# Performance work log

Measured on AMD Instinct MI355X. Metric: run time of the kernel, lower is better.

The kernel has to match this reference:

```python
import jax, jax.numpy as jnp
import numpy as np

LEAKY_SLOPE = 0.2
N, IN_DIM, OUT_DIM = 8192, 128, 64


def setup_inputs() -> dict:
    key = jax.random.key(0)
    k1, k2, k3, k4, k5 = jax.random.split(key, 5)
    X = jax.random.normal(k1, (N, IN_DIM), dtype=jnp.float32)
    A = jax.random.randint(k2, (N, N), 0, 2, dtype=jnp.int32)
    W = jax.random.normal(k3, (IN_DIM, OUT_DIM), dtype=jnp.float32) / np.sqrt(IN_DIM)
    a_l = jax.random.normal(k4, (OUT_DIM,), dtype=jnp.float32) / np.sqrt(OUT_DIM)
    a_r = jax.random.normal(k5, (OUT_DIM,), dtype=jnp.float32) / np.sqrt(OUT_DIM)
    return {"X": X, "A": A, "W": W, "a_l": a_l, "a_r": a_r}


def reference(X, A, W, a_l, a_r):
    # 1) linear transform: H = X @ W  -> [N, out_dim]
    H = X @ W
    # 2) additive attention scores: e_ij = leaky_relu(a_l.H_i + a_r.H_j)
    e_l = H @ a_l  # [N]
    e_r = H @ a_r  # [N]
    e = jax.nn.leaky_relu(e_l[:, None] + e_r[None, :], negative_slope=LEAKY_SLOPE)
    # 3) mask non-edges
    e = jnp.where(A == 0, -jnp.inf, e)
    # 4) row-wise softmax over neighbors j
    alpha = jax.nn.softmax(e, axis=1)
    # 5) weighted aggregation
    return alpha @ H
```

## Files before the change

### kernel.cpp

```cpp
#include <hip/hip_runtime.h>

typedef __attribute__((ext_vector_type(8))) short short8v;
typedef __attribute__((ext_vector_type(4))) float f32x4;
typedef __attribute__((ext_vector_type(2))) unsigned int uint2v;

#define NN 8192
#define HDIM 64
#define KDIM 128
#define LOG2E 1.44269504088896340736f

#if defined(__has_builtin)
#if __has_builtin(__builtin_amdgcn_cvt_pk_fp8_f32) && __has_builtin(__builtin_amdgcn_mfma_f32_16x16x32_fp8_fp8)
#define FP8PATH 1
#endif
#endif

#define PIN() asm volatile("" ::: "memory")
#define BAR() asm volatile("s_waitcnt lgkmcnt(0)\n\ts_barrier" ::: "memory")

__device__ __forceinline__ unsigned short f2b(float f) {
    unsigned int u = __float_as_uint(f);
    return (unsigned short)((u + 0x7fffu + ((u >> 16) & 1u)) >> 16);
}

__global__ __launch_bounds__(256) void gat_prep(
    const float* __restrict__ X, const float* __restrict__ W,
    const float* __restrict__ al, const float* __restrict__ ar,
    void* __restrict__ HbTv, float* __restrict__ el2p,
    float* __restrict__ cpv, float* __restrict__ erp)
{
    __shared__ float Wl[KDIM * HDIM];
    const int t = threadIdx.x;
    {
        const float4* Wv = (const float4*)W;
        float4* Wlv = (float4*)Wl;
#pragma unroll
        for (int s = 0; s < 8; ++s) Wlv[t + s * 256] = Wv[t + s * 256];
    }
    __syncthreads();
    const int row = blockIdx.x * 32 + (t >> 3);
    const int cg = t & 7;
    const int c0 = cg * 8;
    float al8[8], ar8[8];
#pragma unroll
    for (int j = 0; j < 8; ++j) { al8[j] = al[c0 + j]; ar8[j] = ar[c0 + j]; }
    float acc[8];
#pragma unroll
    for (int j = 0; j < 8; ++j) acc[j] = 0.f;
    const float4* Xv = (const float4*)(X + row * KDIM);
    for (int k4 = 0; k4 < 32; ++k4) {
        float4 x4 = Xv[k4];
        float xs[4] = {x4.x, x4.y, x4.z, x4.w};
#pragma unroll
        for (int kk = 0; kk < 4; ++kk) {
            const int k = k4 * 4 + kk;
            const float x = xs[kk];
            const float4 w0 = *(const float4*)&Wl[k * HDIM + c0];
            const float4 w1 = *(const float4*)&Wl[k * HDIM + c0 + 4];
            acc[0] = fmaf(x, w0.x, acc[0]); acc[1] = fmaf(x, w0.y, acc[1]);
            acc[2] = fmaf(x, w0.z, acc[2]); acc[3] = fmaf(x, w0.w, acc[3]);
            acc[4] = fmaf(x, w1.x, acc[4]); acc[5] = fmaf(x, w1.y, acc[5]);
            acc[6] = fmaf(x, w1.z, acc[6]); acc[7] = fmaf(x, w1.w, acc[7]);
        }
    }
    float pl = 0.f, pr = 0.f;
#pragma unroll
    for (int j = 0; j < 8; ++j) {
        pl = fmaf(acc[j], al8[j], pl);
        pr = fmaf(acc[j], ar8[j], pr);
    }
    pl += __shfl_xor(pl, 1, 64); pl += __shfl_xor(pl, 2, 64); pl += __shfl_xor(pl, 4, 64);
    pr += __shfl_xor(pr, 1, 64); pr += __shfl_xor(pr, 2, 64); pr += __shfl_xor(pr, 4, 64);
    if (cg == 0) {
        const float el = pl;
        const float s8 = el + 8.0f;
        const float m = fmaxf(s8, 0.2f * s8);
        el2p[row] = (el - m + 8.0f) * LOG2E;
        cpv[row] = (-0.8f * m + 6.4f) * LOG2E;
        erp[row] = pr * LOG2E;
    }
#ifdef FP8PATH
    unsigned char* HbT8 = (unsigned char*)HbTv;
#pragma unroll
    for (int j = 0; j < 8; ++j) {
        const unsigned int b8 =
            (unsigned int)__builtin_amdgcn_cvt_pk_fp8_f32(acc[j], acc[j], 0, false) & 0xffu;
        HbT8[(long)(c0 + j) * NN + row] = (unsigned char)b8;
    }
#else
    unsigned short* HbT = (unsigned short*)HbTv;
#pragma unroll
    for (int j = 0; j < 8; ++j) HbT[(long)(c0 + j) * NN + row] = f2b(acc[j]);
#endif
}

__global__ __launch_bounds__(256, 4) void gat_main(
    const int* __restrict__ A, const void* __restrict__ HbTv,
    const float* __restrict__ el2p, const float* __restrict__ cpv,
    const float* __restrict__ erp, float* __restrict__ out_part,
    float* __restrict__ dsum_part)
{
    const int t = threadIdx.x;
    const int l = t & 63;
    const int w = t >> 6;
    const int rowbase = (blockIdx.x >> 1) * 16;
    const int jsplit = blockIdx.x & 1;
    const int jq16 = jsplit * 16;
    const int l15 = l & 15, lq = l >> 4;

    float el2c[4], cpc[4];
    const int4* Ap[4];
#pragma unroll
    for (int i = 0; i < 4; ++i) {
        const int gr = rowbase + 4 * i + w;
        el2c[i] = el2p[gr];
        cpc[i] = cpv[gr];
        Ap[i] = (const int4*)(A + (long)gr * NN + 4 * l);
    }
    f32x4 acc = {0.f, 0.f, 0.f, 0.f};
    f32x4 accs = {0.f, 0.f, 0.f, 0.f};
    const bool do_sum = (w == 0);

    int4 A0[4], A1[4];
    float4 E0, E1;

    auto loadT = [&](int4* av, float4& e4, int jt) {
        const int jb4 = jt * 64;
#pragma unroll
        for (int i = 0; i < 4; ++i) av[i] = Ap[i][jb4];
        e4 = *(const float4*)(erp + jt * 256 + 4 * l);
    };

#ifdef FP8PATH
    __shared__ __align__(16) unsigned char plds[2][16 * 264];
    const unsigned char* bbase = (const unsigned char*)HbTv + (long)(w * 16 + l15) * NN + lq * 8;
    const int aoff = l15 * 264 + lq * 8;
    const long long ONES8 = 0x3838383838383838LL;
    unsigned long long Bf[8];

    auto issueB = [&](int jt) {
        const unsigned char* bp = bbase + (long)jt * 256;
#pragma unroll
        for (int kc = 0; kc < 8; ++kc)
            Bf[kc] = *(const unsigned long long*)(bp + kc * 32);
    };

    auto phase1 = [&](const int4* av, const float4 e4, unsigned char* buf) {
        const float e[4] = {e4.x, e4.y, e4.z, e4.w};
#pragma unroll
        for (int i = 0; i < 4; ++i) {
            const int am[4] = {av[i].x, av[i].y, av[i].z, av[i].w};
            float p[4];
#pragma unroll
            for (int c = 0; c < 4; ++c) {
                const float u = el2c[i] + e[c];
                const float v = fmaf(u, 0.2f, cpc[i]);
                float g = fmaxf(u, v);
                g = am[c] ? g : -1e30f;
                p[c] = __builtin_amdgcn_exp2f(g);
            }
            unsigned int pk = (unsigned int)__builtin_amdgcn_cvt_pk_fp8_f32(p[0], p[1], 0, false);
            pk = (unsigned int)__builtin_amdgcn_cvt_pk_fp8_f32(p[2], p[3], (int)pk, true);
            *(unsigned int*)(buf + (4 * i + w) * 264 + 4 * l) = pk;
        }
    };

    auto mfmaT = [&](const unsigned char* buf) {
        __builtin_amdgcn_s_setprio(1);
#pragma unroll
        for (int kc = 0; kc < 8; ++kc) {
            const long long af = *(const long long*)(buf + aoff + kc * 32);
            acc = __builtin_amdgcn_mfma_f32_16x16x32_fp8_fp8(af, (long long)Bf[kc], acc, 0, 0, 0);
            if (do_sum)
                accs = __builtin_amdgcn_mfma_f32_16x16x32_fp8_fp8(af, ONES8, accs, 0, 0, 0);
        }
        __builtin_amdgcn_s_setprio(0);
    };
#else
    __shared__ unsigned short plds[2][16 * 264];
    union { unsigned short s[8]; short8v v; } ones;
#pragma unroll
    for (int i = 0; i < 8; ++i) ones.s[i] = 0x3F80;
    const unsigned short* bbase = (const unsigned short*)HbTv + (long)(w * 16 + l15) * NN + lq * 8;
    const int aoff = l15 * 264 + lq * 8;
    short8v Bf[8];

    auto issueB = [&](int jt) {
        const unsigned short* bp = bbase + (long)jt * 256;
#pragma unroll
        for (int kc = 0; kc < 8; ++kc) Bf[kc] = *(const short8v*)(bp + kc * 32);
    };

    auto phase1 = [&](const int4* av, const float4 e4, unsigned short* buf) {
        const float e[4] = {e4.x, e4.y, e4.z, e4.w};
#pragma unroll
        for (int i = 0; i < 4; ++i) {
            const int am[4] = {av[i].x, av[i].y, av[i].z, av[i].w};
            float p[4];
#pragma unroll
            for (int c = 0; c < 4; ++c) {
                const float u = el2c[i] + e[c];
                const float v = fmaf(u, 0.2f, cpc[i]);
                float g = fmaxf(u, v);
                g = am[c] ? g : -1e30f;
                p[c] = __builtin_amdgcn_exp2f(g);
            }
            const unsigned int lo = (__float_as_uint(p[0]) >> 16) |
                                    (__float_as_uint(p[1]) & 0xffff0000u);
            const unsigned int hi = (__float_as_uint(p[2]) >> 16) |
                                    (__float_as_uint(p[3]) & 0xffff0000u);
            *(uint2v*)(buf + (4 * i + w) * 264 + 4 * l) = (uint2v){lo, hi};
        }
    };

    auto mfmaT = [&](const unsigned short* buf) {
        __builtin_amdgcn_s_setprio(1);
#pragma unroll
        for (int kc = 0; kc < 8; ++kc) {
            short8v af = *(const short8v*)(buf + aoff + kc * 32);
            acc = __builtin_amdgcn_mfma_f32_16x16x32_bf16(af, Bf[kc], acc, 0, 0, 0);
            if (do_sum)
                accs = __builtin_amdgcn_mfma_f32_16x16x32_bf16(af, ones.v, accs, 0, 0, 0);
        }
        __builtin_amdgcn_s_setprio(0);
    };
#endif

    loadT(A0, E0, jq16);
    loadT(A1, E1, jq16 + 1);
#pragma unroll
    for (int s = 0; s < 8; ++s) {
        const int jt = jq16 + 2 * s;
        issueB(jt);
        PIN();
        phase1(A0, E0, plds[0]);
        if (s < 7) loadT(A0, E0, jt + 2);
        BAR();
        mfmaT(plds[0]);
        issueB(jt + 1);
        PIN();
        phase1(A1, E1, plds[1]);
        if (s < 7) loadT(A1, E1, jt + 3);
        BAR();
        mfmaT(plds[1]);
    }

    if (do_sum && l15 == 0)
#pragma unroll
        for (int r = 0; r < 4; ++r)
            dsum_part[(long)jsplit * NN + rowbase + lq * 4 + r] = accs[r];
    float* op = out_part + (long)jsplit * NN * HDIM;
#pragma unroll
    for (int r = 0; r < 4; ++r) {
        const int row = lq * 4 + r;
        op[(long)(rowbase + row) * HDIM + w * 16 + l15] = acc[r];
    }
}

__global__ __launch_bounds__(256) void gat_norm(
    const float* __restrict__ out_part, const float* __restrict__ dsum_part,
    float* __restrict__ out)
{
    const int i4 = blockIdx.x * 256 + threadIdx.x;
    const int row = i4 >> 4;
    const float4* p0 = (const float4*)out_part;
    const float4 v0 = p0[i4];
    const float4 v1 = p0[i4 + (NN * HDIM / 4)];
    const float d = dsum_part[row] + dsum_part[NN + row];
    const float ri = 1.0f / d;
    float4 o;
    o.x = (v0.x + v1.x) * ri;
    o.y = (v0.y + v1.y) * ri;
    o.z = (v0.z + v1.z) * ri;
    o.w = (v0.w + v1.w) * ri;
    ((float4*)out)[i4] = o;
}

extern "C" void kernel_launch(void* const* d_in, const int* in_sizes, int n_in,
                              void* d_out, int out_size, void* d_ws, size_t ws_size,
                              hipStream_t stream) {
    const float *X = nullptr, *W = nullptr, *al = nullptr, *ar = nullptr;
    const int* A = nullptr;
    for (int i = 0; i < n_in; ++i) {
        const long s = in_sizes[i];
        if (s == (long)NN * NN) A = (const int*)d_in[i];
        else if (s == (long)NN * KDIM) X = (const float*)d_in[i];
        else if (s == (long)KDIM * HDIM) W = (const float*)d_in[i];
        else if (s == HDIM) { if (!al) al = (const float*)d_in[i]; else ar = (const float*)d_in[i]; }
    }
    float* out = (float*)d_out;
    void* HbTv = d_ws;
    float* el2p = (float*)((char*)d_ws + (long)NN * HDIM * 2);
    float* cpv = el2p + NN;
    float* erp = cpv + NN;
    float* out_part = erp + NN;
    float* dsum_part = out_part + 2L * NN * HDIM;
    hipLaunchKernelGGL(gat_prep, dim3(256), dim3(256), 0, stream, X, W, al, ar, HbTv, el2p, cpv, erp);
    hipLaunchKernelGGL(gat_main, dim3(1024), dim3(256), 0, stream, A, HbTv, el2p, cpv, erp, out_part, dsum_part);
    hipLaunchKernelGGL(gat_norm, dim3(512), dim3(256), 0, stream, out_part, dsum_part, out);
}
```

Before: 90.23 us.

## Merge two tile phases per barrier with quad-buffered LDS and dual B registers

Restructures the main loop so both phase1 computations for a tile pair run before one barrier, followed by both MFMA groups. To keep this race-free, the LDS P buffer becomes four-way rotating and the B fragments get two register sets. This halves the barriers per iteration and lets more global loads stay in flight, at the cost of twice the LDS use and more live registers, which may reduce occupancy.

```diff
diff --git a/kernel.cpp b/kernel.cpp
--- a/kernel.cpp
+++ b/kernel.cpp
@@ -132,17 +132,21 @@
     };
 
 #ifdef FP8PATH
-    __shared__ __align__(16) unsigned char plds[2][16 * 264];
+    __shared__ __align__(16) unsigned char plds[4][16 * 264];
     const unsigned char* bbase = (const unsigned char*)HbTv + (long)(w * 16 + l15) * NN + lq * 8;
     const int aoff = l15 * 264 + lq * 8;
     const long long ONES8 = 0x3838383838383838LL;
-    unsigned long long Bf[8];
-
-    auto issueB = [&](int jt) {
+    unsigned long long Bfa[8], Bfb[8];
+
+    auto issueBa = [&](int jt) {
         const unsigned char* bp = bbase + (long)jt * 256;
 #pragma unroll
-        for (int kc = 0; kc < 8; ++kc)
-            Bf[kc] = *(const unsigned long long*)(bp + kc * 32);
+        for (int kc = 0; kc < 8; ++kc) Bfa[kc] = *(const unsigned long long*)(bp + kc * 32);
+    };
+    auto issueBb = [&](int jt) {
+        const unsigned char* bp = bbase + (long)jt * 256;
+#pragma unroll
+        for (int kc = 0; kc < 8; ++kc) Bfb[kc] = *(const unsigned long long*)(bp + kc * 32);
     };
 
     auto phase1 = [&](const int4* av, const float4 e4, unsigned char* buf) {
@@ -165,30 +169,46 @@
         }
     };
 
-    auto mfmaT = [&](const unsigned char* buf) {
+    auto mfmaTa = [&](const unsigned char* buf) {
         __builtin_amdgcn_s_setprio(1);
 #pragma unroll
         for (int kc = 0; kc < 8; ++kc) {
             const long long af = *(const long long*)(buf + aoff + kc * 32);
-            acc = __builtin_amdgcn_mfma_f32_16x16x32_fp8_fp8(af, (long long)Bf[kc], acc, 0, 0, 0);
+            acc = __builtin_amdgcn_mfma_f32_16x16x32_fp8_fp8(af, (long long)Bfa[kc], acc, 0, 0, 0);
             if (do_sum)
                 accs = __builtin_amdgcn_mfma_f32_16x16x32_fp8_fp8(af, ONES8, accs, 0, 0, 0);
         }
         __builtin_amdgcn_s_setprio(0);
     };
+    auto mfmaTb = [&](const unsigned char* buf) {
+        __builtin_amdgcn_s_setprio(1);
+#pragma unroll
+        for (int kc = 0; kc < 8; ++kc) {
+            const long long af = *(const long long*)(buf + aoff + kc * 32);
+            acc = __builtin_amdgcn_mfma_f32_16x16x32_fp8_fp8(af, (long long)Bfb[kc], acc, 0, 0, 0);
+            if (do_sum)
+                accs = __builtin_amdgcn_mfma_f32_16x16x32_fp8_fp8(af, ONES8, accs, 0, 0, 0);
+        }
+        __builtin_amdgcn_s_setprio(0);
+    };
 #else
-    __shared__ unsigned short plds[2][16 * 264];
+    __shared__ unsigned short plds[4][16 * 264];
     union { unsigned short s[8]; short8v v; } ones;
 #pragma unroll
     for (int i = 0; i < 8; ++i) ones.s[i] = 0x3F80;
     const unsigned short* bbase = (const unsigned short*)HbTv + (long)(w * 16 + l15) * NN + lq * 8;
     const int aoff = l15 * 264 + lq * 8;
-    short8v Bf[8];
-
-    auto issueB = [&](int jt) {
+    short8v Bfa[8], Bfb[8];
+
+    auto issueBa = [&](int jt) {
         const unsigned short* bp = bbase + (long)jt * 256;
 #pragma unroll
-        for (int kc = 0; kc < 8; ++kc) Bf[kc] = *(const short8v*)(bp + kc * 32);
+        for (int kc = 0; kc < 8; ++kc) Bfa[kc] = *(const short8v*)(bp + kc * 32);
+    };
+    auto issueBb = [&](int jt) {
+        const unsigned short* bp = bbase + (long)jt * 256;
+#pragma unroll
+        for (int kc = 0; kc < 8; ++kc) Bfb[kc] = *(const short8v*)(bp + kc * 32);
     };
 
     auto phase1 = [&](const int4* av, const float4 e4, unsigned short* buf) {
@@ -213,17 +233,28 @@
         }
     };
 
-    auto mfmaT = [&](const unsigned short* buf) {
+    auto mfmaTa = [&](const unsigned short* buf) {
         __builtin_amdgcn_s_setprio(1);
 #pragma unroll
         for (int kc = 0; kc < 8; ++kc) {
             short8v af = *(const short8v*)(buf + aoff + kc * 32);
-            acc = __builtin_amdgcn_mfma_f32_16x16x32_bf16(af, Bf[kc], acc, 0, 0, 0);
+            acc = __builtin_amdgcn_mfma_f32_16x16x32_bf16(af, Bfa[kc], acc, 0, 0, 0);
             if (do_sum)
                 accs = __builtin_amdgcn_mfma_f32_16x16x32_bf16(af, ones.v, accs, 0, 0, 0);
         }
         __builtin_amdgcn_s_setprio(0);
     };
+    auto mfmaTb = [&](const unsigned short* buf) {
+        __builtin_amdgcn_s_setprio(1);
+#pragma unroll
+        for (int kc = 0; kc < 8; ++kc) {
+            short8v af = *(const short8v*)(buf + aoff + kc * 32);
+            acc = __builtin_amdgcn_mfma_f32_16x16x32_bf16(af, Bfb[kc], acc, 0, 0, 0);
+            if (do_sum)
+                accs = __builtin_amdgcn_mfma_f32_16x16x32_bf16(af, ones.v, accs, 0, 0, 0);
+        }
+        __builtin_amdgcn_s_setprio(0);
+    };
 #endif
 
     loadT(A0, E0, jq16);
@@ -231,18 +262,18 @@
 #pragma unroll
     for (int s = 0; s < 8; ++s) {
         const int jt = jq16 + 2 * s;
-        issueB(jt);
+        const int b0 = (2 * s) & 3, b1 = (2 * s + 1) & 3;
+        issueBa(jt);
         PIN();
-        phase1(A0, E0, plds[0]);
+        phase1(A0, E0, plds[b0]);
         if (s < 7) loadT(A0, E0, jt + 2);
-        BAR();
-        mfmaT(plds[0]);
-        issueB(jt + 1);
+        issueBb(jt + 1);
         PIN();
-        phase1(A1, E1, plds[1]);
+        phase1(A1, E1, plds[b1]);
         if (s < 7) loadT(A1, E1, jt + 3);
         BAR();
-        mfmaT(plds[1]);
+        mfmaTa(plds[b0]);
+        mfmaTb(plds[b1]);
     }
 
     if (do_sum && l15 == 0)
```

Result: no change. 89.74 us (-0.5%).
